# Kernel tuning notes

Hardware: AMD Instinct MI355X
Metric: run time of the kernel (lower is better)

The kernel has to match this reference:

```python
import jax, jax.numpy as jnp
import numpy as np

N_NODES = 100000


def gcn_conv(x, edge_index, W, b):
    """PyG GCNConv: h = x W^T; add self-loops; symmetric deg^-1/2 norm; scatter-add; + bias."""
    n = x.shape[0]
    src = jnp.concatenate([edge_index[0], jnp.arange(n)])  # self-loops appended
    dst = jnp.concatenate([edge_index[1], jnp.arange(n)])
    deg = jax.ops.segment_sum(jnp.ones_like(dst, dtype=x.dtype), dst, num_segments=n)
    dinv = jnp.where(deg > 0, jax.lax.rsqrt(deg), 0.0)
    norm = dinv[src] * dinv[dst]                             # [E+n]
    h = x @ W.T                                              # [n, out]
    msg = norm[:, None] * h[src]                             # [E+n, out] gather
    out = jax.ops.segment_sum(msg, dst, num_segments=n)      # scatter-add
    return out + b


def setup_inputs() -> dict:
    key = jax.random.key(0)
    ks = jax.random.split(key, 10)
    input_dim, gnn_hidden, tree_hidden, num_classes = 128, 64, 32, 8
    n_edges = 3200000
    x = jax.random.normal(ks[0], (N_NODES, input_dim), dtype=jnp.float32)
    edge_index = jax.random.randint(ks[1], (2, n_edges), 0, N_NODES, dtype=jnp.int64)
    # GCNConv params (PyG Linear weight is [out, in], glorot-ish scale)
    W1 = jax.random.normal(ks[2], (gnn_hidden, input_dim), dtype=jnp.float32) / np.sqrt(input_dim)
    b1 = jnp.zeros((gnn_hidden,), dtype=jnp.float32)
    W2 = jax.random.normal(ks[3], (tree_hidden, gnn_hidden), dtype=jnp.float32) / np.sqrt(gnn_hidden)
    b2 = jnp.zeros((tree_hidden,), dtype=jnp.float32)
    # SoftDecisionTree params (torch.randn init in source)
    gate_w = jax.random.normal(ks[4], (tree_hidden, tree_hidden), dtype=jnp.float32)
    gate_b = jnp.zeros((tree_hidden,), dtype=jnp.float32)
    leaf_w = jax.random.normal(ks[5], (tree_hidden, num_classes), dtype=jnp.float32)
    return {"x": x, "edge_index": edge_index, "W1": W1, "b1": b1, "W2": W2,
            "b2": b2, "gate_w": gate_w, "gate_b": gate_b, "leaf_w": leaf_w}


def reference(x, edge_index, W1, b1, W2, b2, gate_w, gate_b, leaf_w):
    h = jax.nn.relu(gcn_conv(x, edge_index, W1, b1))
    h = gcn_conv(h, edge_index, W2, b2)
    gates = jax.nn.sigmoid(h @ gate_w.T + gate_b)
    return gates @ leaf_w
```

## Files before the change

### kernel.cpp

```cpp
#include <hip/hip_runtime.h>
#include <math.h>

#define IN_DIM 128
#define H1 64
#define H2 32
#define NC 8
#define SCAN_CH 1024
#define NB_MAX 512
#define BLK 512
#define CAP 12288

typedef unsigned int u32;

__device__ __forceinline__ float bf_lo(u32 u) { return __uint_as_float(u << 16); }
__device__ __forceinline__ float bf_hi(u32 u) { return __uint_as_float(u & 0xffff0000u); }
__device__ __forceinline__ unsigned short f2b(float f) {
  u32 u = __float_as_uint(f);
  u += 0x7fffu + ((u >> 16) & 1u);
  return (unsigned short)(u >> 16);
}


__global__ __launch_bounds__(256) void k_hist(const int* __restrict__ dst,
                                              int* __restrict__ bh,
                                              int E, int EPB, int NBk) {
  __shared__ int h[NB_MAX];
  int k = blockIdx.x, tid = threadIdx.x;
  for (int i = tid; i < NBk; i += 256) h[i] = 0;
  __syncthreads();
  int st = k * EPB, en = min(E, st + EPB);
  for (int i = st + tid; i < en; i += 256)
    atomicAdd(&h[((u32)dst[i]) >> 8], 1);
  __syncthreads();
  for (int b = tid; b < NBk; b += 256) bh[b * BLK + k] = h[b];
}


__global__ __launch_bounds__(256) void k_gsc1(const int* __restrict__ A,
                                              int* __restrict__ bsum, int L) {
  int b = blockIdx.x, tid = threadIdx.x;
  int i0 = b * SCAN_CH + tid * 4;
  int s = 0;
  if (i0 + 3 < L) {
    int4 v = *(const int4*)(A + i0);
    s = v.x + v.y + v.z + v.w;
  } else {
    for (int i = i0; i < L; ++i) s += A[i];
  }
  __shared__ int red[256];
  red[tid] = s;
  __syncthreads();
  for (int d = 128; d > 0; d >>= 1) {
    if (tid < d) red[tid] += red[tid + d];
    __syncthreads();
  }
  if (tid == 0) bsum[b] = red[0];
}

__global__ __launch_bounds__(256) void k_gsc2(const int* __restrict__ bsum,
                                              int* __restrict__ bbase,
                                              int* __restrict__ S, int nbk, int L) {
  __shared__ int part[256];
  int tid = threadIdx.x;
  int chunk = (nbk + 255) / 256;
  int st = tid * chunk, en = min(st + chunk, nbk);
  int s = 0;
  for (int i = st; i < en; ++i) s += bsum[i];
  part[tid] = s;
  __syncthreads();
  for (int d = 1; d < 256; d <<= 1) {
    int t = (tid >= d) ? part[tid - d] : 0;
    __syncthreads();
    part[tid] += t;
    __syncthreads();
  }
  int base = (tid == 0) ? 0 : part[tid - 1];
  for (int i = st; i < en; ++i) { bbase[i] = base; base += bsum[i]; }
  if (tid == 255) S[L] = part[255];
}

__global__ __launch_bounds__(256) void k_gsc3(const int* __restrict__ A,
                                              const int* __restrict__ bbase,
                                              int* __restrict__ S, int L) {
  int b = blockIdx.x, tid = threadIdx.x;
  int i0 = b * SCAN_CH + tid * 4;
  int e0 = 0, e1 = 0, e2 = 0, e3 = 0;
  if (i0 + 3 < L) {
    int4 v = *(const int4*)(A + i0);
    e0 = v.x; e1 = v.y; e2 = v.z; e3 = v.w;
  } else {
    if (i0 + 0 < L) e0 = A[i0 + 0];
    if (i0 + 1 < L) e1 = A[i0 + 1];
    if (i0 + 2 < L) e2 = A[i0 + 2];
    if (i0 + 3 < L) e3 = A[i0 + 3];
  }
  __shared__ int part[256];
  part[tid] = e0 + e1 + e2 + e3;
  __syncthreads();
  for (int d = 1; d < 256; d <<= 1) {
    int t = (tid >= d) ? part[tid - d] : 0;
    __syncthreads();
    part[tid] += t;
    __syncthreads();
  }
  int base = bbase[b] + ((tid == 0) ? 0 : part[tid - 1]);
  int o0 = base, o1 = o0 + e0, o2 = o1 + e1, o3 = o2 + e2;
  if (i0 + 3 < L) {
    int4 o; o.x = o0; o.y = o1; o.z = o2; o.w = o3;
    *(int4*)(S + i0) = o;
  } else {
    if (i0 + 0 < L) S[i0 + 0] = o0;
    if (i0 + 1 < L) S[i0 + 1] = o1;
    if (i0 + 2 < L) S[i0 + 2] = o2;
    if (i0 + 3 < L) S[i0 + 3] = o3;
  }
}


__global__ __launch_bounds__(256) void k_scatter(const int* __restrict__ src,
                                                 const int* __restrict__ dst,
                                                 const int* __restrict__ S,
                                                 u32* __restrict__ packed,
                                                 int E, int EPB, int NBk) {
  __shared__ int cur[NB_MAX];
  int k = blockIdx.x, tid = threadIdx.x;
  for (int b = tid; b < NBk; b += 256) cur[b] = S[b * BLK + k];
  __syncthreads();
  int st = k * EPB, en = min(E, st + EPB);
  for (int i = st + tid; i < en; i += 256) {
    int d = dst[i];
    int b = ((u32)d) >> 8;
    int pos = atomicAdd(&cur[b], 1);
    packed[pos] = (((u32)d & 255u) << 17) | (u32)src[i];
  }
}


__global__ __launch_bounds__(256) void k_build(const u32* __restrict__ packed,
                                               const int* __restrict__ S,
                                               int* __restrict__ csr,
                                               int* __restrict__ off,
                                               float* __restrict__ dinv,
                                               int n, int NBk) {
  __shared__ int cnt[256];
  __shared__ int tmp[256];
  __shared__ int cur[256];
  __shared__ int sbuf[CAP];
  int b = blockIdx.x, tid = threadIdx.x;
  int r0 = S[b * BLK];
  int r1 = S[(b + 1) * BLK];
  int m = r1 - r0;
  cnt[tid] = 0;
  __syncthreads();
  for (int i = r0 + tid; i < r1; i += 256)
    atomicAdd(&cnt[packed[i] >> 17], 1);
  __syncthreads();
  int v = cnt[tid];
  tmp[tid] = v;
  __syncthreads();
  for (int d = 1; d < 256; d <<= 1) {
    int t = (tid >= d) ? tmp[tid - d] : 0;
    __syncthreads();
    tmp[tid] += t;
    __syncthreads();
  }
  int rel = tmp[tid] - v;
  int node = b * 256 + tid;
  if (node < n) {
    off[node] = r0 + rel;
    dinv[node] = rsqrtf((float)(v + 1));
  }
  if (b == NBk - 1 && tid == 0) off[n] = r1;
  cur[tid] = rel;
  __syncthreads();
  if (m <= CAP) {
    for (int i = r0 + tid; i < r1; i += 256) {
      u32 u = packed[i];
      int pos = atomicAdd(&cur[u >> 17], 1);
      sbuf[pos] = (int)(u & 0x1FFFFu);
    }
    __syncthreads();
    for (int j = tid; j < m; j += 256)
      csr[r0 + j] = sbuf[j];
  } else {
    for (int i = r0 + tid; i < r1; i += 256) {
      u32 u = packed[i];
      int pos = atomicAdd(&cur[u >> 17], 1);
      csr[r0 + pos] = (int)(u & 0x1FFFFu);
    }
  }
}


__global__ void k_proj1(const float4* __restrict__ x4, const float* __restrict__ W1,
                        const float* __restrict__ dinv,
                        unsigned short* __restrict__ h1p, int n) {
  __shared__ float xs[16][IN_DIM];
  __shared__ float wt[IN_DIM][H1 + 1];
  int tid = threadIdx.x;
  int row0 = blockIdx.x * 16;

  for (int i = tid; i < (H1 * IN_DIM / 4); i += 256) {
    float4 w = ((const float4*)W1)[i];
    int o = (i * 4) / IN_DIM;
    int k = (i * 4) % IN_DIM;
    wt[k + 0][o] = w.x; wt[k + 1][o] = w.y; wt[k + 2][o] = w.z; wt[k + 3][o] = w.w;
  }
  for (int i = tid; i < 16 * IN_DIM / 4; i += 256) {
    int r = (i * 4) / IN_DIM, k = (i * 4) % IN_DIM;
    int row = row0 + r;
    if (row < n)
      *((float4*)&xs[r][k]) = x4[(size_t)row * (IN_DIM / 4) + k / 4];
  }
  __syncthreads();

  int o = tid & 63, rq = tid >> 6;
  float a0 = 0.f, a1 = 0.f, a2 = 0.f, a3 = 0.f;
  for (int k = 0; k < IN_DIM; ++k) {
    float w = wt[k][o];
    a0 += xs[rq * 4 + 0][k] * w;
    a1 += xs[rq * 4 + 1][k] * w;
    a2 += xs[rq * 4 + 2][k] * w;
    a3 += xs[rq * 4 + 3][k] * w;
  }
  int r = row0 + rq * 4;
  if (r + 0 < n) h1p[(size_t)(r + 0) * H1 + o] = f2b(a0 * dinv[r + 0]);
  if (r + 1 < n) h1p[(size_t)(r + 1) * H1 + o] = f2b(a1 * dinv[r + 1]);
  if (r + 2 < n) h1p[(size_t)(r + 2) * H1 + o] = f2b(a2 * dinv[r + 2]);
  if (r + 3 < n) h1p[(size_t)(r + 3) * H1 + o] = f2b(a3 * dinv[r + 3]);
}


#define ACC8(v) do { \
    a0 += bf_lo((v).x); a1 += bf_hi((v).x); \
    a2 += bf_lo((v).y); a3 += bf_hi((v).y); \
    a4 += bf_lo((v).z); a5 += bf_hi((v).z); \
    a6 += bf_lo((v).w); a7 += bf_hi((v).w); } while (0)

#define RED8(m) do { \
    a0 += __shfl_xor(a0, m, 64); a1 += __shfl_xor(a1, m, 64); \
    a2 += __shfl_xor(a2, m, 64); a3 += __shfl_xor(a3, m, 64); \
    a4 += __shfl_xor(a4, m, 64); a5 += __shfl_xor(a5, m, 64); \
    a6 += __shfl_xor(a6, m, 64); a7 += __shfl_xor(a7, m, 64); } while (0)

__global__ __launch_bounds__(256) void k_agg64_proj2(
    const u32* __restrict__ hp,
    const float* __restrict__ dinv,
    const int* __restrict__ off, const int* __restrict__ csr,
    const float* __restrict__ b1, const float* __restrict__ W2,
    unsigned short* __restrict__ h2p, int n) {
  __shared__ float wt[H1][H2 + 1];
  __shared__ float rows[4][H1];
  __shared__ float b1s[H1];
  int tid = threadIdx.x;

  for (int i = tid; i < H2 * H1 / 4; i += 256) {
    float4 w = ((const float4*)W2)[i];
    int o = (i * 4) / H1, k = (i * 4) % H1;
    wt[k + 0][o] = w.x; wt[k + 1][o] = w.y; wt[k + 2][o] = w.z; wt[k + 3][o] = w.w;
  }
  if (tid < 16) ((float4*)b1s)[tid] = ((const float4*)b1)[tid];
  __syncthreads();

  int lane = tid & 63;
  int wv = __builtin_amdgcn_readfirstlane(tid >> 6);
  int wid0 = blockIdx.x * 4 + wv;
  int wid = wid0 < n ? wid0 : n - 1;
  int g = lane >> 3, j = lane & 7;

  const uint4* __restrict__ hp4 = (const uint4*)hp;
  float a0 = 0.f, a1 = 0.f, a2 = 0.f, a3 = 0.f,
        a4 = 0.f, a5 = 0.f, a6 = 0.f, a7 = 0.f;

  if (g == 0) {
    uint4 v = hp4[(size_t)wid * (H1 / 8) + j];
    ACC8(v);
  }
  int r0 = off[wid], r1 = off[wid + 1];
  for (int base = r0; base < r1; base += 32) {
    int ci = base + (lane & 31);
    int s = csr[min(ci, r1 - 1)];
#pragma unroll
    for (int it = 0; it < 4; ++it) {
      int sv = __shfl(s, it * 8 + g, 64);
      if (base + it * 8 + g < r1) {
        uint4 v = hp4[(size_t)sv * (H1 / 8) + j];
        ACC8(v);
      }
    }
  }
  RED8(8); RED8(16); RED8(32);

  float d = dinv[wid];
  if (lane < 8) {
    float4 v0, v1;
    v0.x = fmaxf(a0 * d + b1s[8 * lane + 0], 0.f);
    v0.y = fmaxf(a1 * d + b1s[8 * lane + 1], 0.f);
    v0.z = fmaxf(a2 * d + b1s[8 * lane + 2], 0.f);
    v0.w = fmaxf(a3 * d + b1s[8 * lane + 3], 0.f);
    v1.x = fmaxf(a4 * d + b1s[8 * lane + 4], 0.f);
    v1.y = fmaxf(a5 * d + b1s[8 * lane + 5], 0.f);
    v1.z = fmaxf(a6 * d + b1s[8 * lane + 6], 0.f);
    v1.w = fmaxf(a7 * d + b1s[8 * lane + 7], 0.f);
    *(float4*)&rows[wv][8 * lane + 0] = v0;
    *(float4*)&rows[wv][8 * lane + 4] = v1;
  }
  __syncthreads();

  int half = lane >> 5, o = lane & 31;
  float a = 0.f;
#pragma unroll
  for (int k = 0; k < 32; ++k) {
    int kk = half * 32 + k;
    a += rows[wv][kk] * wt[kk][o];
  }
  a += __shfl_down(a, 32, 64);
  if (half == 0 && wid0 < n) h2p[(size_t)wid0 * H2 + o] = f2b(a * d);
}


__global__ __launch_bounds__(256) void k_agg32_tree(
    const u32* __restrict__ hp,
    const float* __restrict__ dinv,
    const int* __restrict__ off, const int* __restrict__ csr,
    const float* __restrict__ b2, const float* __restrict__ gate_w,
    const float* __restrict__ gate_b, const float* __restrict__ leaf_w,
    float* __restrict__ out, int n) {
  __shared__ float gwt[H2][H2 + 1];
  __shared__ float lws[H2][NC + 1];
  __shared__ float rowh[4][H2];
  __shared__ float rowg[4][H2];
  __shared__ float b2s[H2];
  int tid = threadIdx.x;

  {
    float4 w = ((const float4*)gate_w)[tid];
    int jj = (tid * 4) / H2, k = (tid * 4) % H2;
    gwt[k + 0][jj] = w.x; gwt[k + 1][jj] = w.y; gwt[k + 2][jj] = w.z; gwt[k + 3][jj] = w.w;
  }
  lws[tid >> 3][tid & 7] = leaf_w[tid];
  if (tid < 8) ((float4*)b2s)[tid] = ((const float4*)b2)[tid];
  __syncthreads();

  int lane = tid & 63;
  int wv = __builtin_amdgcn_readfirstlane(tid >> 6);
  int wid0 = blockIdx.x * 4 + wv;
  int wid = wid0 < n ? wid0 : n - 1;
  int g = lane >> 2, j = lane & 3;

  const uint4* __restrict__ hp4 = (const uint4*)hp;
  float a0 = 0.f, a1 = 0.f, a2 = 0.f, a3 = 0.f,
        a4 = 0.f, a5 = 0.f, a6 = 0.f, a7 = 0.f;

  if (g == 0) {
    uint4 v = hp4[(size_t)wid * (H2 / 8) + j];
    ACC8(v);
  }
  int r0 = off[wid], r1 = off[wid + 1];
  for (int base = r0; base < r1; base += 32) {
    int ci = base + (lane & 31);
    int s = csr[min(ci, r1 - 1)];
#pragma unroll
    for (int it = 0; it < 2; ++it) {
      int sv = __shfl(s, it * 16 + g, 64);
      if (base + it * 16 + g < r1) {
        uint4 v = hp4[(size_t)sv * (H2 / 8) + j];
        ACC8(v);
      }
    }
  }
  RED8(4); RED8(8); RED8(16); RED8(32);

  float d = dinv[wid];
  if (lane < 4) {
    float4 v0, v1;
    v0.x = a0 * d + b2s[8 * lane + 0];
    v0.y = a1 * d + b2s[8 * lane + 1];
    v0.z = a2 * d + b2s[8 * lane + 2];
    v0.w = a3 * d + b2s[8 * lane + 3];
    v1.x = a4 * d + b2s[8 * lane + 4];
    v1.y = a5 * d + b2s[8 * lane + 5];
    v1.z = a6 * d + b2s[8 * lane + 6];
    v1.w = a7 * d + b2s[8 * lane + 7];
    *(float4*)&rowh[wv][8 * lane + 0] = v0;
    *(float4*)&rowh[wv][8 * lane + 4] = v1;
  }
  __syncthreads();

  int half = lane >> 5, f = lane & 31;
  float gacc = 0.f;
#pragma unroll
  for (int k = 0; k < 16; ++k) {
    int kk = half * 16 + k;
    gacc += rowh[wv][kk] * gwt[kk][f];
  }
  gacc += __shfl_down(gacc, 32, 64);
  if (half == 0) rowg[wv][f] = 1.0f / (1.0f + __expf(-(gacc + gate_b[f])));
  __syncthreads();

  int c = lane & 7, gi = lane >> 3;
  float a = 0.f;
#pragma unroll
  for (int j4 = 0; j4 < 4; ++j4) {
    int jj = gi * 4 + j4;
    a += rowg[wv][jj] * lws[jj][c];
  }
  a += __shfl_down(a, 32, 64);
  a += __shfl_down(a, 16, 64);
  a += __shfl_down(a, 8, 64);
  if (lane < 8 && wid0 < n) out[(size_t)wid0 * NC + lane] = a;
}


extern "C" void kernel_launch(void* const* d_in, const int* in_sizes, int n_in,
                              void* d_out, int out_size, void* d_ws, size_t ws_size,
                              hipStream_t stream) {
  const float* x  = (const float*)d_in[0];
  const int*   ei = (const int*)d_in[1];
  const float* W1 = (const float*)d_in[2];
  const float* b1 = (const float*)d_in[3];
  const float* W2 = (const float*)d_in[4];
  const float* b2 = (const float*)d_in[5];
  const float* gw = (const float*)d_in[6];
  const float* gb = (const float*)d_in[7];
  const float* lw = (const float*)d_in[8];
  float* out = (float*)d_out;

  int n = in_sizes[0] / IN_DIM;
  int E = in_sizes[1] / 2;
  const int* src  = ei;
  const int* dstp = ei + E;

  int NBk = (n + 255) >> 8;
  int EPB = (E + BLK - 1) / BLK;
  int L   = NBk * BLK;
  int nbs = (L + SCAN_CH - 1) / SCAN_CH;

  size_t n4  = ((size_t)n + 3) & ~(size_t)3;
  size_t np4 = ((size_t)n + 1 + 3) & ~(size_t)3;
  size_t E4  = ((size_t)E + 3) & ~(size_t)3;
  size_t L4  = ((size_t)L + 1 + 3) & ~(size_t)3;
  size_t nbs4 = ((size_t)nbs + 3) & ~(size_t)3;
  char* w = (char*)d_ws;
  int* csr    = (int*)w;   w += E4 * 4;
  u32* packed = (u32*)w;   w += E4 * 4;
  int* bh     = (int*)w;   w += L4 * 4;
  int* S      = (int*)w;   w += L4 * 4;
  int* bsum   = (int*)w;   w += nbs4 * 4;
  int* bbase  = (int*)w;   w += nbs4 * 4;
  float* dinv = (float*)w; w += n4 * 4;
  int* off    = (int*)w;   w += np4 * 4;
  unsigned short* h1p = (unsigned short*)w;  w += n4 * (size_t)H1 * 2;
  unsigned short* h2p = (unsigned short*)w;

  int gw4 = (n + 3) / 4;

  k_hist<<<BLK, 256, 0, stream>>>(dstp, bh, E, EPB, NBk);
  k_gsc1<<<nbs, 256, 0, stream>>>(bh, bsum, L);
  k_gsc2<<<1, 256, 0, stream>>>(bsum, bbase, S, nbs, L);
  k_gsc3<<<nbs, 256, 0, stream>>>(bh, bbase, S, L);
  k_scatter<<<BLK, 256, 0, stream>>>(src, dstp, S, packed, E, EPB, NBk);
  k_build<<<NBk, 256, 0, stream>>>(packed, S, csr, off, dinv, n, NBk);

  k_proj1<<<(n + 15) / 16, 256, 0, stream>>>((const float4*)x, W1, dinv, h1p, n);
  k_agg64_proj2<<<gw4, 256, 0, stream>>>((const u32*)h1p, dinv, off, csr, b1, W2, h2p, n);
  k_agg32_tree<<<gw4, 256, 0, stream>>>((const u32*)h2p, dinv, off, csr, b2, gw, gb, lw, out, n);
}
```

Measured before the change: 412.2 us.

## Split layer-1 aggregation into two 32-column passes to shrink gather footprint

```diff
diff --git a/kernel.cpp b/kernel.cpp
--- a/kernel.cpp
+++ b/kernel.cpp
@@ -194,7 +194,8 @@
 
 __global__ void k_proj1(const float4* __restrict__ x4, const float* __restrict__ W1,
                         const float* __restrict__ dinv,
-                        unsigned short* __restrict__ h1p, int n) {
+                        unsigned short* __restrict__ h1p0,
+                        unsigned short* __restrict__ h1p1, int n) {
   __shared__ float xs[16][IN_DIM];
   __shared__ float wt[IN_DIM][H1 + 1];
   int tid = threadIdx.x;
@@ -223,11 +224,12 @@
     a2 += xs[rq * 4 + 2][k] * w;
     a3 += xs[rq * 4 + 3][k] * w;
   }
+  unsigned short* hb = (o < 32) ? (h1p0 + o) : (h1p1 + (o - 32));
   int r = row0 + rq * 4;
-  if (r + 0 < n) h1p[(size_t)(r + 0) * H1 + o] = f2b(a0 * dinv[r + 0]);
-  if (r + 1 < n) h1p[(size_t)(r + 1) * H1 + o] = f2b(a1 * dinv[r + 1]);
-  if (r + 2 < n) h1p[(size_t)(r + 2) * H1 + o] = f2b(a2 * dinv[r + 2]);
-  if (r + 3 < n) h1p[(size_t)(r + 3) * H1 + o] = f2b(a3 * dinv[r + 3]);
+  if (r + 0 < n) hb[(size_t)(r + 0) * 32] = f2b(a0 * dinv[r + 0]);
+  if (r + 1 < n) hb[(size_t)(r + 1) * 32] = f2b(a1 * dinv[r + 1]);
+  if (r + 2 < n) hb[(size_t)(r + 2) * 32] = f2b(a2 * dinv[r + 2]);
+  if (r + 3 < n) hb[(size_t)(r + 3) * 32] = f2b(a3 * dinv[r + 3]);
 }
 
 
@@ -243,37 +245,40 @@
     a4 += __shfl_xor(a4, m, 64); a5 += __shfl_xor(a5, m, 64); \
     a6 += __shfl_xor(a6, m, 64); a7 += __shfl_xor(a7, m, 64); } while (0)
 
-__global__ __launch_bounds__(256) void k_agg64_proj2(
-    const u32* __restrict__ hp,
+template <int PASS>
+__global__ __launch_bounds__(256) void k_agg64_half(
+    const u32* __restrict__ hpH,
     const float* __restrict__ dinv,
     const int* __restrict__ off, const int* __restrict__ csr,
-    const float* __restrict__ b1, const float* __restrict__ W2,
-    unsigned short* __restrict__ h2p, int n) {
+    const float* __restrict__ b1,
+    float* __restrict__ agg0,
+    const float* __restrict__ W2,
+    unsigned short* __restrict__ h2p,
+    int n) {
   __shared__ float wt[H1][H2 + 1];
   __shared__ float rows[4][H1];
-  __shared__ float b1s[H1];
   int tid = threadIdx.x;
 
-  for (int i = tid; i < H2 * H1 / 4; i += 256) {
-    float4 w = ((const float4*)W2)[i];
-    int o = (i * 4) / H1, k = (i * 4) % H1;
-    wt[k + 0][o] = w.x; wt[k + 1][o] = w.y; wt[k + 2][o] = w.z; wt[k + 3][o] = w.w;
-  }
-  if (tid < 16) ((float4*)b1s)[tid] = ((const float4*)b1)[tid];
-  __syncthreads();
+  if (PASS == 1) {
+    for (int i = tid; i < H2 * H1 / 4; i += 256) {
+      float4 w = ((const float4*)W2)[i];
+      int o = (i * 4) / H1, k = (i * 4) % H1;
+      wt[k + 0][o] = w.x; wt[k + 1][o] = w.y; wt[k + 2][o] = w.z; wt[k + 3][o] = w.w;
+    }
+  }
 
   int lane = tid & 63;
   int wv = __builtin_amdgcn_readfirstlane(tid >> 6);
   int wid0 = blockIdx.x * 4 + wv;
   int wid = wid0 < n ? wid0 : n - 1;
-  int g = lane >> 3, j = lane & 7;
-
-  const uint4* __restrict__ hp4 = (const uint4*)hp;
+  int g = lane >> 2, j = lane & 3;
+
+  const uint4* __restrict__ hp4 = (const uint4*)hpH;
   float a0 = 0.f, a1 = 0.f, a2 = 0.f, a3 = 0.f,
         a4 = 0.f, a5 = 0.f, a6 = 0.f, a7 = 0.f;
 
   if (g == 0) {
-    uint4 v = hp4[(size_t)wid * (H1 / 8) + j];
+    uint4 v = hp4[(size_t)wid * 4 + j];
     ACC8(v);
   }
   int r0 = off[wid], r1 = off[wid + 1];
@@ -281,41 +286,62 @@
     int ci = base + (lane & 31);
     int s = csr[min(ci, r1 - 1)];
 #pragma unroll
-    for (int it = 0; it < 4; ++it) {
-      int sv = __shfl(s, it * 8 + g, 64);
-      if (base + it * 8 + g < r1) {
-        uint4 v = hp4[(size_t)sv * (H1 / 8) + j];
+    for (int it = 0; it < 2; ++it) {
+      int sv = __shfl(s, it * 16 + g, 64);
+      if (base + it * 16 + g < r1) {
+        uint4 v = hp4[(size_t)sv * 4 + j];
         ACC8(v);
       }
     }
   }
-  RED8(8); RED8(16); RED8(32);
+  RED8(4); RED8(8); RED8(16); RED8(32);
 
   float d = dinv[wid];
-  if (lane < 8) {
-    float4 v0, v1;
-    v0.x = fmaxf(a0 * d + b1s[8 * lane + 0], 0.f);
-    v0.y = fmaxf(a1 * d + b1s[8 * lane + 1], 0.f);
-    v0.z = fmaxf(a2 * d + b1s[8 * lane + 2], 0.f);
-    v0.w = fmaxf(a3 * d + b1s[8 * lane + 3], 0.f);
-    v1.x = fmaxf(a4 * d + b1s[8 * lane + 4], 0.f);
-    v1.y = fmaxf(a5 * d + b1s[8 * lane + 5], 0.f);
-    v1.z = fmaxf(a6 * d + b1s[8 * lane + 6], 0.f);
-    v1.w = fmaxf(a7 * d + b1s[8 * lane + 7], 0.f);
-    *(float4*)&rows[wv][8 * lane + 0] = v0;
-    *(float4*)&rows[wv][8 * lane + 4] = v1;
-  }
-  __syncthreads();
-
-  int half = lane >> 5, o = lane & 31;
-  float a = 0.f;
+  if (PASS == 0) {
+    if (lane < 4 && wid0 < n) {
+      float4 v0, v1;
+      v0.x = fmaxf(a0 * d + b1[8 * lane + 0], 0.f);
+      v0.y = fmaxf(a1 * d + b1[8 * lane + 1], 0.f);
+      v0.z = fmaxf(a2 * d + b1[8 * lane + 2], 0.f);
+      v0.w = fmaxf(a3 * d + b1[8 * lane + 3], 0.f);
+      v1.x = fmaxf(a4 * d + b1[8 * lane + 4], 0.f);
+      v1.y = fmaxf(a5 * d + b1[8 * lane + 5], 0.f);
+      v1.z = fmaxf(a6 * d + b1[8 * lane + 6], 0.f);
+      v1.w = fmaxf(a7 * d + b1[8 * lane + 7], 0.f);
+      *(float4*)&agg0[(size_t)wid0 * 32 + 8 * lane + 0] = v0;
+      *(float4*)&agg0[(size_t)wid0 * 32 + 8 * lane + 4] = v1;
+    }
+  } else {
+    if (lane < 4) {
+      const float* bb = b1 + 32;
+      float4 v0, v1;
+      v0.x = fmaxf(a0 * d + bb[8 * lane + 0], 0.f);
+      v0.y = fmaxf(a1 * d + bb[8 * lane + 1], 0.f);
+      v0.z = fmaxf(a2 * d + bb[8 * lane + 2], 0.f);
+      v0.w = fmaxf(a3 * d + bb[8 * lane + 3], 0.f);
+      v1.x = fmaxf(a4 * d + bb[8 * lane + 4], 0.f);
+      v1.y = fmaxf(a5 * d + bb[8 * lane + 5], 0.f);
+      v1.z = fmaxf(a6 * d + bb[8 * lane + 6], 0.f);
+      v1.w = fmaxf(a7 * d + bb[8 * lane + 7], 0.f);
+      *(float4*)&rows[wv][32 + 8 * lane + 0] = v0;
+      *(float4*)&rows[wv][32 + 8 * lane + 4] = v1;
+    }
+    if (lane < 8) {
+      float4 t = ((const float4*)(agg0 + (size_t)wid * 32))[lane];
+      *(float4*)&rows[wv][4 * lane] = t;
+    }
+    __syncthreads();
+
+    int half = lane >> 5, o = lane & 31;
+    float a = 0.f;
 #pragma unroll
-  for (int k = 0; k < 32; ++k) {
-    int kk = half * 32 + k;
-    a += rows[wv][kk] * wt[kk][o];
-  }
-  a += __shfl_down(a, 32, 64);
-  if (half == 0 && wid0 < n) h2p[(size_t)wid0 * H2 + o] = f2b(a * d);
+    for (int k = 0; k < 32; ++k) {
+      int kk = half * 32 + k;
+      a += rows[wv][kk] * wt[kk][o];
+    }
+    a += __shfl_down(a, 32, 64);
+    if (half == 0 && wid0 < n) h2p[(size_t)wid0 * H2 + o] = f2b(a * d);
+  }
 }
 
 
@@ -450,8 +476,11 @@
   int* bbase  = (int*)w;   w += nbs4 * 4;
   float* dinv = (float*)w; w += n4 * 4;
   int* off    = (int*)w;   w += np4 * 4;
-  unsigned short* h1p = (unsigned short*)w;  w += n4 * (size_t)H1 * 2;
-  unsigned short* h2p = (unsigned short*)w;
+  unsigned short* h1p0 = (unsigned short*)w;  w += n4 * 32 * 2;
+  unsigned short* h1p1 = (unsigned short*)w;  w += n4 * 32 * 2;
+  unsigned short* h2p  = (unsigned short*)w;
+
+  float* agg0 = (float*)packed;
 
   int gw4 = (n + 3) / 4;
 
@@ -462,7 +491,10 @@
   k_scatter<<<BLK, 256, 0, stream>>>(src, dstp, S, packed, E, EPB, NBk);
   k_build<<<NBk, 256, 0, stream>>>(packed, S, csr, off, dinv, n, NBk);
 
-  k_proj1<<<(n + 15) / 16, 256, 0, stream>>>((const float4*)x, W1, dinv, h1p, n);
-  k_agg64_proj2<<<gw4, 256, 0, stream>>>((const u32*)h1p, dinv, off, csr, b1, W2, h2p, n);
+  k_proj1<<<(n + 15) / 16, 256, 0, stream>>>((const float4*)x, W1, dinv, h1p0, h1p1, n);
+  k_agg64_half<0><<<gw4, 256, 0, stream>>>((const u32*)h1p0, dinv, off, csr, b1,
+                                           agg0, nullptr, nullptr, n);
+  k_agg64_half<1><<<gw4, 256, 0, stream>>>((const u32*)h1p1, dinv, off, csr, b1,
+                                           agg0, W2, h2p, n);
   k_agg32_tree<<<gw4, 256, 0, stream>>>((const u32*)h2p, dinv, off, csr, b2, gw, gb, lw, out, n);
 }
```

After: 427.4 us. +3.7%, slower.
